# Performance work log

Hardware: AMD Instinct MI355X
Metric: run time of the kernel (lower is better)

Reference implementation:

```python
import jax, jax.numpy as jnp
import numpy as np

N_NODES = 50000
N_EDGES = 800000
D = 128
N_LAYERS = 5
N_REL = 500
N_ENT = 50000  # fc output size (num_entities)
BATCH = 1024


def setup_inputs() -> dict:
    key = jax.random.key(0)
    ks = jax.random.split(key, 10)
    return {
        "entity_embed": jax.random.normal(ks[0], (N_NODES, D), dtype=jnp.float32),
        "edge_val": jnp.ones((N_EDGES,), dtype=jnp.float32),
        "gnn_W": jax.random.normal(ks[1], (N_LAYERS, D, D), dtype=jnp.float32) * (1.0 / np.sqrt(D)),
        "gnn_b": jax.random.normal(ks[2], (N_LAYERS, D), dtype=jnp.float32) * 0.01,
        "rel_table": jax.random.normal(ks[3], (N_REL, D), dtype=jnp.float32),
        "fc_W": jax.random.normal(ks[4], (2 * D, N_ENT), dtype=jnp.float32) * (1.0 / np.sqrt(2 * D)),
        "fc_b": jax.random.normal(ks[5], (N_ENT,), dtype=jnp.float32) * 0.01,
        "edge_row": jax.random.randint(ks[6], (N_EDGES,), 0, N_NODES, dtype=jnp.int32),
        "edge_col": jax.random.randint(ks[7], (N_EDGES,), 0, N_NODES, dtype=jnp.int32),
        "head_idx": jax.random.randint(ks[8], (BATCH,), 0, N_NODES, dtype=jnp.int32),
        "rel_ids": jax.random.randint(ks[9], (BATCH,), 0, N_REL, dtype=jnp.int32),
    }


def reference(entity_embed, edge_val, gnn_W, gnn_b, rel_table, fc_W, fc_b,
              edge_row, edge_col, head_idx, rel_ids):
    n_nodes = entity_embed.shape[0]

    def layer(x, wb):
        W, b = wb
        # sparse.mm(adj, x): out[row] += val * x[col]
        msgs = edge_val[:, None] * x[edge_col]          # [E, D]
        agg = jax.ops.segment_sum(msgs, edge_row, num_segments=n_nodes)  # [N, D]
        return jax.nn.relu(agg @ W + b), None

    all_embed, _ = jax.lax.scan(layer, entity_embed, (gnn_W, gnn_b))

    head_embed = all_embed[head_idx]                    # [B, D]
    rel_embed = rel_table[rel_ids]                      # [B, D]
    embed = jnp.concatenate([head_embed, rel_embed], axis=1)  # [B, 2D]
    logits = embed @ fc_W + fc_b                        # [B, N_ENT]
    return logits
```

## Files before the change

### kernel.cpp

```cpp
#include <hip/hip_runtime.h>


#define N_NODES 50000
#define N_EDGES 800000
#define D 128
#define N_LAYERS 5
#define N_ENT 50000
#define BATCH 1024
#define KDIM 256
#define SCAN_BLOCKS ((N_NODES + 255) / 256)
#define FC_NT 128

typedef __attribute__((ext_vector_type(8))) __bf16 bf16x8;
typedef __attribute__((ext_vector_type(4))) float f32x4;
typedef __attribute__((ext_vector_type(8))) unsigned short u16x8;
typedef __attribute__((ext_vector_type(4))) unsigned short u16x4;

__device__ inline unsigned short f2bf(float x) {
  unsigned int u = __float_as_uint(x);
  unsigned int r = (u + 0x7FFFu + ((u >> 16) & 1u)) >> 16;
  return (unsigned short)r;
}
__device__ inline float bf2f(unsigned short b) {
  return __uint_as_float(((unsigned int)b) << 16);
}

__global__ void zero_i32(int* __restrict__ p, int n) {
  int i = blockIdx.x * blockDim.x + threadIdx.x;
  if (i < n) p[i] = 0;
}

__global__ void hist_kernel(const int* __restrict__ rows, int* __restrict__ counts) {
  int i = blockIdx.x * blockDim.x + threadIdx.x;
  int stride = gridDim.x * blockDim.x;
  for (; i < N_EDGES; i += stride) atomicAdd(&counts[rows[i]], 1);
}

__device__ inline int block_exscan256(int v, int* wsum, int* tot) {
  int t = threadIdx.x, lane = t & 63, wid = t >> 6;
  int s = v;
#pragma unroll
  for (int off = 1; off < 64; off <<= 1) {
    int u = __shfl_up(s, off, 64);
    if (lane >= off) s += u;
  }
  if (lane == 63) wsum[wid] = s;
  __syncthreads();
  if (t == 0) {
    int run = 0;
#pragma unroll
    for (int w = 0; w < 4; ++w) { int tmp = wsum[w]; wsum[w] = run; run += tmp; }
    wsum[4] = run;
  }
  __syncthreads();
  *tot = wsum[4];
  return wsum[wid] + s - v;
}

__global__ __launch_bounds__(256) void scan1_kernel(const int* __restrict__ counts,
                                                    int* __restrict__ row_ptr,
                                                    int* __restrict__ bsum) {
  __shared__ int wsum[5];
  int i = blockIdx.x * 256 + threadIdx.x;
  int v = (i < N_NODES) ? counts[i] : 0;
  int tot;
  int ex = block_exscan256(v, wsum, &tot);
  if (i < N_NODES) row_ptr[i] = ex;
  if (threadIdx.x == 0) bsum[blockIdx.x] = tot;
}

__global__ __launch_bounds__(256) void scan2_kernel(int* __restrict__ bsum) {
  __shared__ int wsum[5];
  int t = threadIdx.x;
  int v = (t < SCAN_BLOCKS) ? bsum[t] : 0;
  int tot;
  int ex = block_exscan256(v, wsum, &tot);
  if (t < SCAN_BLOCKS) bsum[t] = ex;
}

__global__ __launch_bounds__(256) void scan3_kernel(const int* __restrict__ counts,
                                                    const int* __restrict__ bsum,
                                                    int* __restrict__ row_ptr,
                                                    int* __restrict__ cursor) {
  int i = blockIdx.x * 256 + threadIdx.x;
  if (i >= N_NODES) return;
  int ex = row_ptr[i] + bsum[blockIdx.x];
  row_ptr[i] = ex;
  cursor[i] = ex;
  if (i == N_NODES - 1) row_ptr[N_NODES] = ex + counts[i];
}

__global__ void scatter_kernel(const int* __restrict__ rows, const int* __restrict__ cols,
                               const float* __restrict__ vals, int* __restrict__ cursor,
                               int* __restrict__ col_s, float* __restrict__ val_s) {
  int i = blockIdx.x * blockDim.x + threadIdx.x;
  int stride = gridDim.x * blockDim.x;
  for (; i < N_EDGES; i += stride) {
    int r = rows[i];
    int pos = atomicAdd(&cursor[r], 1);
    col_s[pos] = cols[i];
    val_s[pos] = vals[i];
  }
}

__global__ __launch_bounds__(256) void tobf16_kernel(const float* __restrict__ src,
                                                     unsigned short* __restrict__ dst,
                                                     int n8) {
  int i = blockIdx.x * blockDim.x + threadIdx.x;
  if (i >= n8) return;
  float4 a = *(const float4*)&src[i * 8];
  float4 b = *(const float4*)&src[i * 8 + 4];
  u16x8 o;
  o[0] = f2bf(a.x); o[1] = f2bf(a.y); o[2] = f2bf(a.z); o[3] = f2bf(a.w);
  o[4] = f2bf(b.x); o[5] = f2bf(b.y); o[6] = f2bf(b.z); o[7] = f2bf(b.w);
  *(u16x8*)&dst[i * 8] = o;
}

__global__ void wconv_kernel(const float* __restrict__ gW, unsigned short* __restrict__ Wt5) {
  int idx = blockIdx.x * 256 + threadIdx.x;
  if (idx >= N_LAYERS * D * D) return;
  int l = idx / (D * D);
  int rem = idx - l * D * D;
  int j = rem >> 7;
  int k = rem & 127;
  Wt5[idx] = f2bf(gW[l * D * D + k * D + j]);
}

__device__ inline void agg_batch(int cl, float vl, int cnt, int q, int l16,
                                 const unsigned short* __restrict__ xb, float* acc) {
  int j = 0;
  for (; j + 4 <= cnt; j += 4) {
    int c[4]; float v[4]; u16x8 xv[4];
#pragma unroll
    for (int u = 0; u < 4; ++u) {
      c[u] = __shfl(cl, q * 16 + j + u);
      v[u] = __shfl(vl, q * 16 + j + u);
    }
#pragma unroll
    for (int u = 0; u < 4; ++u) xv[u] = *(const u16x8*)&xb[c[u] * D + l16 * 8];
#pragma unroll
    for (int u = 0; u < 4; ++u)
#pragma unroll
      for (int dd = 0; dd < 8; ++dd) acc[dd] = fmaf(v[u], bf2f(xv[u][dd]), acc[dd]);
  }
  for (; j < cnt; ++j) {
    int c = __shfl(cl, q * 16 + j);
    float v = __shfl(vl, q * 16 + j);
    u16x8 xv0 = *(const u16x8*)&xb[c * D + l16 * 8];
#pragma unroll
    for (int dd = 0; dd < 8; ++dd) acc[dd] = fmaf(v, bf2f(xv0[dd]), acc[dd]);
  }
}

__global__ __launch_bounds__(256) void layer_fused(const unsigned short* __restrict__ xb,
                                                   const int* __restrict__ row_ptr,
                                                   const int* __restrict__ cols,
                                                   const float* __restrict__ vals,
                                                   const unsigned short* __restrict__ Bt,
                                                   const float* __restrict__ bias,
                                                   unsigned short* __restrict__ yb) {
  __shared__ unsigned short atile[64 * D];
  int t = threadIdx.x, lane = t & 63, wave = t >> 6;
  int q = lane >> 4, l16 = lane & 15;
  int r0 = blockIdx.x * 64;
  char* ab = (char*)atile;

#pragma unroll
  for (int p = 0; p < 4; ++p) {
    int row_l = wave * 16 + p * 4 + q;
    int r = r0 + row_l;
    float acc[8] = {0.f, 0.f, 0.f, 0.f, 0.f, 0.f, 0.f, 0.f};
    if (r < N_NODES) {
      int e0 = row_ptr[r], e1 = row_ptr[r + 1];
      for (int base = e0; base < e1; base += 16) {
        int idx = base + l16;
        bool ok = idx < e1;
        int cl = ok ? cols[idx] : 0;
        float vl = ok ? vals[idx] : 0.f;
        agg_batch(cl, vl, min(16, e1 - base), q, l16, xb, acc);
      }
    }
    u16x8 o;
#pragma unroll
    for (int dd = 0; dd < 8; ++dd) o[dd] = f2bf(acc[dd]);
    *(u16x8*)(ab + row_l * 256 + ((l16 ^ (row_l & 7)) << 4)) = o;
  }
  __syncthreads();

  int lq = lane >> 4;
  f32x4 acc2[4][2];
#pragma unroll
  for (int m = 0; m < 4; ++m) { acc2[m][0] = (f32x4){0,0,0,0}; acc2[m][1] = (f32x4){0,0,0,0}; }
#pragma unroll
  for (int kk = 0; kk < 4; ++kk) {
    bf16x8 wfr[2];
#pragma unroll
    for (int nt = 0; nt < 2; ++nt)
      wfr[nt] = *(const bf16x8*)&Bt[(wave * 32 + nt * 16 + l16) * D + kk * 32 + lq * 8];
#pragma unroll
    for (int m = 0; m < 4; ++m) {
      int row_l = m * 16 + l16;
      bf16x8 afr = *(const bf16x8*)(ab + row_l * 256 + ((((kk * 4 + lq) ^ (row_l & 7)) << 4)));
      acc2[m][0] = __builtin_amdgcn_mfma_f32_16x16x32_bf16(wfr[0], afr, acc2[m][0], 0, 0, 0);
      acc2[m][1] = __builtin_amdgcn_mfma_f32_16x16x32_bf16(wfr[1], afr, acc2[m][1], 0, 0, 0);
    }
  }
#pragma unroll
  for (int nt = 0; nt < 2; ++nt) {
    int jb = wave * 32 + nt * 16 + lq * 4;
    float4 bb = *(const float4*)&bias[jb];
#pragma unroll
    for (int m = 0; m < 4; ++m) {
      int r = r0 + m * 16 + l16;
      if (r < N_NODES) {
        u16x4 o;
        o[0] = f2bf(fmaxf(acc2[m][nt][0] + bb.x, 0.f));
        o[1] = f2bf(fmaxf(acc2[m][nt][1] + bb.y, 0.f));
        o[2] = f2bf(fmaxf(acc2[m][nt][2] + bb.z, 0.f));
        o[3] = f2bf(fmaxf(acc2[m][nt][3] + bb.w, 0.f));
        *(u16x4*)&yb[(size_t)r * D + jb] = o;
      }
    }
  }
}

__global__ __launch_bounds__(256) void layer_head(const unsigned short* __restrict__ xb,
                                                  const int* __restrict__ row_ptr,
                                                  const int* __restrict__ cols,
                                                  const float* __restrict__ vals,
                                                  const int* __restrict__ head_idx,
                                                  const unsigned short* __restrict__ Bt,
                                                  const float* __restrict__ bias,
                                                  unsigned short* __restrict__ ebf) {
  __shared__ unsigned short atile[64 * D];
  int t = threadIdx.x, lane = t & 63, wave = t >> 6;
  int q = lane >> 4, l16 = lane & 15;
  int r0 = blockIdx.x * 64;
  char* ab = (char*)atile;

#pragma unroll
  for (int p = 0; p < 4; ++p) {
    int row_l = wave * 16 + p * 4 + q;
    int b = r0 + row_l;
    int r = head_idx[b];
    float acc[8] = {0.f, 0.f, 0.f, 0.f, 0.f, 0.f, 0.f, 0.f};
    int e0 = row_ptr[r], e1 = row_ptr[r + 1];
    for (int base = e0; base < e1; base += 16) {
      int idx = base + l16;
      bool ok = idx < e1;
      int cl = ok ? cols[idx] : 0;
      float vl = ok ? vals[idx] : 0.f;
      agg_batch(cl, vl, min(16, e1 - base), q, l16, xb, acc);
    }
    u16x8 o;
#pragma unroll
    for (int dd = 0; dd < 8; ++dd) o[dd] = f2bf(acc[dd]);
    *(u16x8*)(ab + row_l * 256 + ((l16 ^ (row_l & 7)) << 4)) = o;
  }
  __syncthreads();

  int lq = lane >> 4;
  f32x4 acc2[4][2];
#pragma unroll
  for (int m = 0; m < 4; ++m) { acc2[m][0] = (f32x4){0,0,0,0}; acc2[m][1] = (f32x4){0,0,0,0}; }
#pragma unroll
  for (int kk = 0; kk < 4; ++kk) {
    bf16x8 wfr[2];
#pragma unroll
    for (int nt = 0; nt < 2; ++nt)
      wfr[nt] = *(const bf16x8*)&Bt[(wave * 32 + nt * 16 + l16) * D + kk * 32 + lq * 8];
#pragma unroll
    for (int m = 0; m < 4; ++m) {
      int row_l = m * 16 + l16;
      bf16x8 afr = *(const bf16x8*)(ab + row_l * 256 + ((((kk * 4 + lq) ^ (row_l & 7)) << 4)));
      acc2[m][0] = __builtin_amdgcn_mfma_f32_16x16x32_bf16(wfr[0], afr, acc2[m][0], 0, 0, 0);
      acc2[m][1] = __builtin_amdgcn_mfma_f32_16x16x32_bf16(wfr[1], afr, acc2[m][1], 0, 0, 0);
    }
  }
#pragma unroll
  for (int nt = 0; nt < 2; ++nt) {
    int jb = wave * 32 + nt * 16 + lq * 4;
    float4 bb = *(const float4*)&bias[jb];
#pragma unroll
    for (int m = 0; m < 4; ++m) {
      int b = r0 + m * 16 + l16;
      u16x4 o;
      o[0] = f2bf(fmaxf(acc2[m][nt][0] + bb.x, 0.f));
      o[1] = f2bf(fmaxf(acc2[m][nt][1] + bb.y, 0.f));
      o[2] = f2bf(fmaxf(acc2[m][nt][2] + bb.z, 0.f));
      o[3] = f2bf(fmaxf(acc2[m][nt][3] + bb.w, 0.f));
      *(u16x4*)&ebf[(size_t)b * KDIM + jb] = o;
    }
  }
}

__global__ __launch_bounds__(128) void rel_fill(const float* __restrict__ rel_table,
                                                const int* __restrict__ rel_ids,
                                                unsigned short* __restrict__ ebf) {
  int b = blockIdx.x;
  int k = threadIdx.x;
  ebf[(size_t)b * KDIM + D + k] = f2bf(rel_table[rel_ids[b] * D + k]);
}

__global__ __launch_bounds__(256) void wt_kernel(const float* __restrict__ fcW,
                                                 unsigned short* __restrict__ Wt) {
  int n = blockIdx.x * 256 + threadIdx.x;
  int k0 = blockIdx.y * 8;
  if (n >= N_ENT) return;
  u16x8 pk;
#pragma unroll
  for (int e = 0; e < 8; ++e) pk[e] = f2bf(fcW[(size_t)(k0 + e) * N_ENT + n]);
  *(u16x8*)&Wt[(size_t)n * KDIM + k0] = pk;
}

__global__ __launch_bounds__(256, 2) void fc_mfma(const unsigned short* __restrict__ ebf,
                                                  const unsigned short* __restrict__ Wt,
                                                  const float* __restrict__ fcb,
                                                  float* __restrict__ out) {
  __shared__ unsigned short etile[64 * KDIM];
  int t = threadIdx.x;
  int lane = t & 63, wave = t >> 6;
  int l16 = lane & 15, lq = lane >> 4;
  int n0 = blockIdx.x * FC_NT;
  char* eb = (char*)etile;

  bf16x8 afr[2][8];
#pragma unroll
  for (int nt = 0; nt < 2; ++nt) {
    const unsigned short* wp = Wt + (size_t)(n0 + wave * 32 + nt * 16 + l16) * KDIM + lq * 8;
#pragma unroll
    for (int kk = 0; kk < 8; ++kk) afr[nt][kk] = *(const bf16x8*)(wp + kk * 32);
  }

  int n_st[2]; float4 bv[2];
#pragma unroll
  for (int nt = 0; nt < 2; ++nt) {
    n_st[nt] = n0 + wave * 32 + nt * 16 + lq * 4;
    bv[nt] = make_float4(0.f, 0.f, 0.f, 0.f);
    if (n_st[nt] < N_ENT) bv[nt] = *(const float4*)&fcb[n_st[nt]];
  }

  for (int bc = 0; bc < 8; ++bc) {
    int b0 = blockIdx.y * 512 + bc * 64;
    const char* esrc = (const char*)(ebf + (size_t)b0 * KDIM);
#pragma unroll
    for (int it = 0; it < 8; ++it) {
      int c = it * 256 + t;
      int row = c >> 5;
      int ci = c & 31;
      float4 v = *(const float4*)(esrc + (size_t)c * 16);
      *(float4*)(eb + row * 512 + ((ci ^ ((row & 7) << 2)) << 4)) = v;
    }
    __syncthreads();

    f32x4 acc[2][4];
#pragma unroll
    for (int nt = 0; nt < 2; ++nt)
#pragma unroll
      for (int m = 0; m < 4; ++m) acc[nt][m] = (f32x4){0.f, 0.f, 0.f, 0.f};

#pragma unroll
    for (int m = 0; m < 4; ++m) {
      int row = m * 16 + l16;
#pragma unroll
      for (int kk = 0; kk < 8; ++kk) {
        bf16x8 bfr = *(const bf16x8*)(eb + row * 512 + ((((kk * 4 + lq) ^ ((row & 7) << 2)) << 4)));
        acc[0][m] = __builtin_amdgcn_mfma_f32_16x16x32_bf16(afr[0][kk], bfr, acc[0][m], 0, 0, 0);
        acc[1][m] = __builtin_amdgcn_mfma_f32_16x16x32_bf16(afr[1][kk], bfr, acc[1][m], 0, 0, 0);
      }
    }

#pragma unroll
    for (int nt = 0; nt < 2; ++nt) {
      if (n_st[nt] < N_ENT) {
#pragma unroll
        for (int m = 0; m < 4; ++m) {
          int b = b0 + m * 16 + l16;
          float4 o = {acc[nt][m][0] + bv[nt].x, acc[nt][m][1] + bv[nt].y,
                      acc[nt][m][2] + bv[nt].z, acc[nt][m][3] + bv[nt].w};
          *(float4*)&out[(size_t)b * N_ENT + n_st[nt]] = o;
        }
      }
    }
    __syncthreads();
  }
}

extern "C" void kernel_launch(void* const* d_in, const int* in_sizes, int n_in,
                              void* d_out, int out_size, void* d_ws, size_t ws_size,
                              hipStream_t stream) {
  const float* entity    = (const float*)d_in[0];
  const float* edge_val  = (const float*)d_in[1];
  const float* gnn_W     = (const float*)d_in[2];
  const float* gnn_b     = (const float*)d_in[3];
  const float* rel_table = (const float*)d_in[4];
  const float* fc_W      = (const float*)d_in[5];
  const float* fc_b      = (const float*)d_in[6];
  const int* edge_row    = (const int*)d_in[7];
  const int* edge_col    = (const int*)d_in[8];
  const int* head_idx    = (const int*)d_in[9];
  const int* rel_ids     = (const int*)d_in[10];
  float* out = (float*)d_out;

  char* ws = (char*)d_ws;
  size_t off = 0;
  auto alloc = [&](size_t bytes) -> void* {
    void* p = ws + off;
    off = (off + bytes + 255) & ~(size_t)255;
    return p;
  };
  int* counts   = (int*)alloc((size_t)N_NODES * 4);
  int* row_ptr  = (int*)alloc((size_t)(N_NODES + 1) * 4);
  int* cursor   = (int*)alloc((size_t)N_NODES * 4);
  int* bsum     = (int*)alloc((size_t)256 * 4);
  int* col_s    = (int*)alloc((size_t)N_EDGES * 4);
  float* val_s  = (float*)alloc((size_t)N_EDGES * 4);
  unsigned short* xA    = (unsigned short*)alloc((size_t)N_NODES * D * 2);
  unsigned short* xB    = (unsigned short*)alloc((size_t)N_NODES * D * 2);
  unsigned short* entbf = (unsigned short*)alloc((size_t)N_NODES * D * 2);
  unsigned short* ebf   = (unsigned short*)alloc((size_t)BATCH * KDIM * 2);
  unsigned short* Wt    = (unsigned short*)alloc((size_t)(N_ENT + 256) * KDIM * 2);
  unsigned short* Wt5   = (unsigned short*)alloc((size_t)N_LAYERS * D * D * 2);

  zero_i32<<<(N_NODES + 255) / 256, 256, 0, stream>>>(counts, N_NODES);
  hist_kernel<<<1024, 256, 0, stream>>>(edge_row, counts);
  scan1_kernel<<<SCAN_BLOCKS, 256, 0, stream>>>(counts, row_ptr, bsum);
  scan2_kernel<<<1, 256, 0, stream>>>(bsum);
  scan3_kernel<<<SCAN_BLOCKS, 256, 0, stream>>>(counts, bsum, row_ptr, cursor);
  scatter_kernel<<<1024, 256, 0, stream>>>(edge_row, edge_col, edge_val, cursor, col_s, val_s);

  tobf16_kernel<<<(N_NODES * D / 8 + 255) / 256, 256, 0, stream>>>(entity, entbf, N_NODES * D / 8);
  wconv_kernel<<<(N_LAYERS * D * D + 255) / 256, 256, 0, stream>>>(gnn_W, Wt5);

  for (int layer = 0; layer < N_LAYERS - 1; ++layer) {
    const unsigned short* xin = (layer == 0) ? entbf : ((layer & 1) ? xA : xB);
    unsigned short* yout = (layer & 1) ? xB : xA;
    layer_fused<<<(N_NODES + 63) / 64, 256, 0, stream>>>(xin, row_ptr, col_s, val_s,
                                                         Wt5 + (size_t)layer * D * D,
                                                         gnn_b + (size_t)layer * D, yout);
  }

  dim3 wtg((N_ENT + 255) / 256, KDIM / 8);
  wt_kernel<<<wtg, 256, 0, stream>>>(fc_W, Wt);

  layer_head<<<BATCH / 64, 256, 0, stream>>>(xB, row_ptr, col_s, val_s, head_idx,
                                             Wt5 + (size_t)(N_LAYERS - 1) * D * D,
                                             gnn_b + (size_t)(N_LAYERS - 1) * D, ebf);
  rel_fill<<<BATCH, 128, 0, stream>>>(rel_table, rel_ids, ebf);

  dim3 fcg((N_ENT + FC_NT - 1) / FC_NT, 2);
  fc_mfma<<<fcg, 256, 0, stream>>>(ebf, Wt, fc_b, out);
}
```

Measured before the change: 385.2 us.

## Prune layer four to neighbours of head nodes via mask and compaction

Layer four's output is only read by the final head layer at the in-neighbours of the batch head nodes. The change marks those nodes, compacts them with a prefix scan into a row list, and runs a pruned layer kernel only over that list instead of all 50000 nodes. This removes most of one full aggregation and GEMM layer, at the cost of several small extra launches for marking, scanning and compacting. The pruned kernel still launches the full grid and has blocks past the count exit early.

Result: no change. 392.2 us (+1.8%).

```diff
diff --git a/kernel.cpp b/kernel.cpp
--- a/kernel.cpp
+++ b/kernel.cpp
@@ -101,6 +101,29 @@
     col_s[pos] = cols[i];
     val_s[pos] = vals[i];
   }
+}
+
+__global__ __launch_bounds__(256) void mark_kernel(const int* __restrict__ head_idx,
+                                                   const int* __restrict__ row_ptr,
+                                                   const int* __restrict__ cols,
+                                                   int* __restrict__ mask) {
+  int b = blockIdx.x * blockDim.x + threadIdx.x;
+  if (b >= BATCH) return;
+  int r = head_idx[b];
+  int e0 = row_ptr[r], e1 = row_ptr[r + 1];
+  for (int e = e0; e < e1; ++e) mask[cols[e]] = 1;
+}
+
+__global__ __launch_bounds__(256) void compact_kernel(const int* __restrict__ mask,
+                                                      const int* __restrict__ mpos,
+                                                      const int* __restrict__ msum,
+                                                      int* __restrict__ rlist,
+                                                      int* __restrict__ cnt) {
+  int i = blockIdx.x * 256 + threadIdx.x;
+  if (i >= N_NODES) return;
+  int pos = mpos[i] + msum[blockIdx.x];
+  if (mask[i]) rlist[pos] = i;
+  if (i == N_NODES - 1) cnt[0] = pos + mask[i];
 }
 
 __global__ __launch_bounds__(256) void tobf16_kernel(const float* __restrict__ src,
@@ -213,6 +236,85 @@
     for (int m = 0; m < 4; ++m) {
       int r = r0 + m * 16 + l16;
       if (r < N_NODES) {
+        u16x4 o;
+        o[0] = f2bf(fmaxf(acc2[m][nt][0] + bb.x, 0.f));
+        o[1] = f2bf(fmaxf(acc2[m][nt][1] + bb.y, 0.f));
+        o[2] = f2bf(fmaxf(acc2[m][nt][2] + bb.z, 0.f));
+        o[3] = f2bf(fmaxf(acc2[m][nt][3] + bb.w, 0.f));
+        *(u16x4*)&yb[(size_t)r * D + jb] = o;
+      }
+    }
+  }
+}
+
+__global__ __launch_bounds__(256) void layer_pruned(const unsigned short* __restrict__ xb,
+                                                    const int* __restrict__ row_ptr,
+                                                    const int* __restrict__ cols,
+                                                    const float* __restrict__ vals,
+                                                    const int* __restrict__ rlist,
+                                                    const int* __restrict__ cnt,
+                                                    const unsigned short* __restrict__ Bt,
+                                                    const float* __restrict__ bias,
+                                                    unsigned short* __restrict__ yb) {
+  int M = cnt[0];
+  int r0 = blockIdx.x * 64;
+  if (r0 >= M) return;
+
+  __shared__ unsigned short atile[64 * D];
+  int t = threadIdx.x, lane = t & 63, wave = t >> 6;
+  int q = lane >> 4, l16 = lane & 15;
+  char* ab = (char*)atile;
+
+#pragma unroll
+  for (int p = 0; p < 4; ++p) {
+    int row_l = wave * 16 + p * 4 + q;
+    int idx = r0 + row_l;
+    float acc[8] = {0.f, 0.f, 0.f, 0.f, 0.f, 0.f, 0.f, 0.f};
+    if (idx < M) {
+      int r = rlist[idx];
+      int e0 = row_ptr[r], e1 = row_ptr[r + 1];
+      for (int base = e0; base < e1; base += 16) {
+        int eidx = base + l16;
+        bool ok = eidx < e1;
+        int cl = ok ? cols[eidx] : 0;
+        float vl = ok ? vals[eidx] : 0.f;
+        agg_batch(cl, vl, min(16, e1 - base), q, l16, xb, acc);
+      }
+    }
+    u16x8 o;
+#pragma unroll
+    for (int dd = 0; dd < 8; ++dd) o[dd] = f2bf(acc[dd]);
+    *(u16x8*)(ab + row_l * 256 + ((l16 ^ (row_l & 7)) << 4)) = o;
+  }
+  __syncthreads();
+
+  int lq = lane >> 4;
+  f32x4 acc2[4][2];
+#pragma unroll
+  for (int m = 0; m < 4; ++m) { acc2[m][0] = (f32x4){0,0,0,0}; acc2[m][1] = (f32x4){0,0,0,0}; }
+#pragma unroll
+  for (int kk = 0; kk < 4; ++kk) {
+    bf16x8 wfr[2];
+#pragma unroll
+    for (int nt = 0; nt < 2; ++nt)
+      wfr[nt] = *(const bf16x8*)&Bt[(wave * 32 + nt * 16 + l16) * D + kk * 32 + lq * 8];
+#pragma unroll
+    for (int m = 0; m < 4; ++m) {
+      int row_l = m * 16 + l16;
+      bf16x8 afr = *(const bf16x8*)(ab + row_l * 256 + ((((kk * 4 + lq) ^ (row_l & 7)) << 4)));
+      acc2[m][0] = __builtin_amdgcn_mfma_f32_16x16x32_bf16(wfr[0], afr, acc2[m][0], 0, 0, 0);
+      acc2[m][1] = __builtin_amdgcn_mfma_f32_16x16x32_bf16(wfr[1], afr, acc2[m][1], 0, 0, 0);
+    }
+  }
+#pragma unroll
+  for (int nt = 0; nt < 2; ++nt) {
+    int jb = wave * 32 + nt * 16 + lq * 4;
+    float4 bb = *(const float4*)&bias[jb];
+#pragma unroll
+    for (int m = 0; m < 4; ++m) {
+      int idx = r0 + m * 16 + l16;
+      if (idx < M) {
+        int r = rlist[idx];
         u16x4 o;
         o[0] = f2bf(fmaxf(acc2[m][nt][0] + bb.x, 0.f));
         o[1] = f2bf(fmaxf(acc2[m][nt][1] + bb.y, 0.f));
@@ -415,6 +517,11 @@
   int* bsum     = (int*)alloc((size_t)256 * 4);
   int* col_s    = (int*)alloc((size_t)N_EDGES * 4);
   float* val_s  = (float*)alloc((size_t)N_EDGES * 4);
+  int* mask     = (int*)alloc((size_t)N_NODES * 4);
+  int* mpos     = (int*)alloc((size_t)N_NODES * 4);
+  int* msum     = (int*)alloc((size_t)256 * 4);
+  int* rlist    = (int*)alloc((size_t)N_NODES * 4);
+  int* cnt      = (int*)alloc((size_t)256 * 4);
   unsigned short* xA    = (unsigned short*)alloc((size_t)N_NODES * D * 2);
   unsigned short* xB    = (unsigned short*)alloc((size_t)N_NODES * D * 2);
   unsigned short* entbf = (unsigned short*)alloc((size_t)N_NODES * D * 2);
@@ -429,10 +536,16 @@
   scan3_kernel<<<SCAN_BLOCKS, 256, 0, stream>>>(counts, bsum, row_ptr, cursor);
   scatter_kernel<<<1024, 256, 0, stream>>>(edge_row, edge_col, edge_val, cursor, col_s, val_s);
 
+  zero_i32<<<(N_NODES + 255) / 256, 256, 0, stream>>>(mask, N_NODES);
+  mark_kernel<<<(BATCH + 255) / 256, 256, 0, stream>>>(head_idx, row_ptr, col_s, mask);
+  scan1_kernel<<<SCAN_BLOCKS, 256, 0, stream>>>(mask, mpos, msum);
+  scan2_kernel<<<1, 256, 0, stream>>>(msum);
+  compact_kernel<<<SCAN_BLOCKS, 256, 0, stream>>>(mask, mpos, msum, rlist, cnt);
+
   tobf16_kernel<<<(N_NODES * D / 8 + 255) / 256, 256, 0, stream>>>(entity, entbf, N_NODES * D / 8);
   wconv_kernel<<<(N_LAYERS * D * D + 255) / 256, 256, 0, stream>>>(gnn_W, Wt5);
 
-  for (int layer = 0; layer < N_LAYERS - 1; ++layer) {
+  for (int layer = 0; layer < 3; ++layer) {
     const unsigned short* xin = (layer == 0) ? entbf : ((layer & 1) ? xA : xB);
     unsigned short* yout = (layer & 1) ? xB : xA;
     layer_fused<<<(N_NODES + 63) / 64, 256, 0, stream>>>(xin, row_ptr, col_s, val_s,
@@ -440,12 +553,16 @@
                                                          gnn_b + (size_t)layer * D, yout);
   }
 
+  layer_pruned<<<(N_NODES + 63) / 64, 256, 0, stream>>>(xA, row_ptr, col_s, val_s, rlist, cnt,
+                                                        Wt5 + (size_t)3 * D * D,
+                                                        gnn_b + (size_t)3 * D, xB);
+
   dim3 wtg((N_ENT + 255) / 256, KDIM / 8);
   wt_kernel<<<wtg, 256, 0, stream>>>(fc_W, Wt);
 
   layer_head<<<BATCH / 64, 256, 0, stream>>>(xB, row_ptr, col_s, val_s, head_idx,
-                                             Wt5 + (size_t)(N_LAYERS - 1) * D * D,
-                                             gnn_b + (size_t)(N_LAYERS - 1) * D, ebf);
+                                             Wt5 + (size_t)4 * D * D,
+                                             gnn_b + (size_t)4 * D, ebf);
   rel_fill<<<BATCH, 128, 0, stream>>>(rel_table, rel_ids, ebf);
 
   dim3 fcg((N_ENT + FC_NT - 1) / FC_NT, 2);
```
